# Kernel tuning notes

Hardware: AMD Instinct MI355X
Metric: run time of the kernel (lower is better)

The kernel has to match this reference:

```python
import jax, jax.numpy as jnp
import numpy as np

B, T, C = 4, 2048, 1024
H, HS = 16, 64


def setup_inputs() -> dict:
    key = jax.random.key(0)
    ks = jax.random.split(key, 5)
    scale = (H * C) ** (-0.5)
    x = jax.random.normal(ks[0], (B, T, C), dtype=jnp.float32)
    Wk = jax.random.normal(ks[1], (H, C, HS), dtype=jnp.float32) * scale
    Wq = jax.random.normal(ks[2], (H, C, HS), dtype=jnp.float32) * scale
    Wv = jax.random.normal(ks[3], (H, C, HS), dtype=jnp.float32) * scale
    proj_w = jax.random.normal(ks[4], (C, C), dtype=jnp.float32) / C ** 0.5
    proj_b = jnp.zeros((C,), dtype=jnp.float32)
    return {"x": x, "Wk": Wk, "Wq": Wq, "Wv": Wv, "proj_w": proj_w, "proj_b": proj_b}


def reference(x, Wk, Wq, Wv, proj_w, proj_b):
    b, t, c = x.shape
    # per-head projections: (B,T,C) x (H,C,D) -> (B,H,T,D)
    q = jnp.einsum('btc,hcd->bhtd', x, Wq)
    k = jnp.einsum('btc,hcd->bhtd', x, Wk)
    v = jnp.einsum('btc,hcd->bhtd', x, Wv)
    # NOTE: original module does not scale by 1/sqrt(head_size)
    wei = jnp.einsum('bhtd,bhsd->bhts', q, k)  # (B,H,T,T)
    causal = jnp.tril(jnp.ones((t, t), dtype=bool))
    wei = jnp.where(causal, wei, -jnp.inf)
    wei = jax.nn.softmax(wei, axis=-1)
    out = jnp.einsum('bhts,bhsd->bhtd', wei, v)
    out = out.transpose(0, 2, 1, 3).reshape(b, t, c)  # concat heads
    return out @ proj_w + proj_b
```

## Files before the change

kernel.cpp:

```cpp
#include <hip/hip_runtime.h>

typedef unsigned short u16;
typedef u16 u16x4 __attribute__((ext_vector_type(4)));
typedef u16 u16x8 __attribute__((ext_vector_type(8)));
typedef unsigned u32x2 __attribute__((ext_vector_type(2)));
typedef __bf16 bf16x8 __attribute__((ext_vector_type(8)));
typedef float f32x4 __attribute__((ext_vector_type(4)));

#define DEV static __device__ __forceinline__

DEV u16 f2bf(float f) {
  union { float f; unsigned u; } v; v.f = f;
  return (u16)((v.u + 0x7FFFu + ((v.u >> 16) & 1u)) >> 16);
}

DEV unsigned pack2(float a, float b) {
  unsigned ua = __builtin_bit_cast(unsigned, a) + 0x8000u;
  unsigned ub = __builtin_bit_cast(unsigned, b) + 0x8000u;
  return (ua >> 16) | (ub & 0xFFFF0000u);
}

DEV void async16(const void* g, void* l) {
  __builtin_amdgcn_global_load_lds((const __attribute__((address_space(1))) void*)g,
                                   (__attribute__((address_space(3))) void*)l, 16, 0, 0);
}

DEV f32x4 mfma16(bf16x8 a, bf16x8 b, f32x4 c) {
  return __builtin_amdgcn_mfma_f32_16x16x32_bf16(a, b, c, 0, 0, 0);
}

DEV float exp2fast(float x) { return __builtin_amdgcn_exp2f(x); }

#define BARRIER() asm volatile("s_barrier" ::: "memory")
#define SB0() __builtin_amdgcn_sched_barrier(0)

__global__ __launch_bounds__(256) void k_prep(const float* __restrict__ x,
                                              const float* __restrict__ Wk,
                                              const float* __restrict__ Wq,
                                              const float* __restrict__ Wv,
                                              const float* __restrict__ pw,
                                              u16* __restrict__ xb,
                                              u16* __restrict__ wT,
                                              u16* __restrict__ pwT) {
  __shared__ float t[64 * 72];
  const int bid = blockIdx.x, tid = threadIdx.x;
  if (bid < 8192) {
    int i = bid * 1024 + tid * 4;
    float4 v = *(const float4*)(x + i);
    u16x4 o = { f2bf(v.x), f2bf(v.y), f2bf(v.z), f2bf(v.w) };
    *(u16x4*)(xb + i) = o;
    return;
  }
  const int role = bid - 8192;
  const float* src;
  u16* dst;
  int rows, cols, bx, by, bz;
  float scale;
  if (role < 768) {
    const int w = role >> 8, rem = role & 255;
    src = (w == 0) ? Wq : ((w == 1) ? Wk : Wv);
    dst = wT + (size_t)w * 1024 * 1024;
    scale = (w == 0) ? 1.44269504088896340736f : 1.0f;
    rows = 1024; cols = 64; bx = 0; by = rem >> 4; bz = rem & 15;
  } else {
    const int p = role - 768;
    src = pw; dst = pwT; scale = 1.0f;
    rows = 1024; cols = 1024; bx = p & 15; by = p >> 4; bz = 0;
  }
  src += (size_t)bz * rows * cols;
  dst += (size_t)bz * rows * cols;
  const int c0 = bx * 64, r0 = by * 64;
  const int rr = tid >> 2, cb = (tid & 3) * 16;
  const float* s = src + (size_t)(r0 + rr) * cols + c0 + cb;
  float4 v0 = *(const float4*)(s + 0);
  float4 v1 = *(const float4*)(s + 4);
  float4 v2 = *(const float4*)(s + 8);
  float4 v3 = *(const float4*)(s + 12);
  *(float4*)(t + rr * 72 + cb + 0)  = v0;
  *(float4*)(t + rr * 72 + cb + 4)  = v1;
  *(float4*)(t + rr * 72 + cb + 8)  = v2;
  *(float4*)(t + rr * 72 + cb + 12) = v3;
  __syncthreads();
  const int dd = tid >> 2, eb = (tid & 3) * 16;
  u16x8 o0, o1;
#pragma unroll
  for (int e = 0; e < 8; ++e) o0[e] = f2bf(t[(eb + e) * 72 + dd] * scale);
#pragma unroll
  for (int e = 0; e < 8; ++e) o1[e] = f2bf(t[(eb + 8 + e) * 72 + dd] * scale);
  u16* dp = dst + (size_t)(c0 + dd) * rows + r0 + eb;
  *(u16x8*)dp = o0;
  *(u16x8*)(dp + 8) = o1;
}

template <int MODE>
__global__ __launch_bounds__(512, 2) void k_gemm(const u16* __restrict__ A,
                                                 const u16* __restrict__ Bt,
                                                 u16* __restrict__ qd,
                                                 u16* __restrict__ kd,
                                                 u16* __restrict__ vd,
                                                 float* __restrict__ out,
                                                 const float* __restrict__ bias) {
  __shared__ u16 lds[3 * 24576];
  const int tid = threadIdx.x;
  const int w = tid >> 6, lane = tid & 63;
  const int quad = lane >> 4, l15 = lane & 15;
  const int wm = w >> 1, wn = w & 1;

  const int gx = (int)gridDim.x;
  int lin = (int)blockIdx.y * gx + (int)blockIdx.x;
  const int nwg = gx * (int)gridDim.y;
  lin = (lin & 7) * (nwg >> 3) + (lin >> 3);
  const size_t mb = (size_t)(lin / gx);
  const int nb = lin % gx;

  const int lr = lane >> 3;
  const int lc = ((lane & 7) ^ lr) << 3;
  const u16* ga0 = A  + (mb * 256 + (size_t)(w * 8 + lr)) * 1024 + lc;
  const u16* gb0 = Bt + ((size_t)nb * 128 + (size_t)(w * 8 + lr)) * 1024 + lc;

  const int swz0 = ((0 + quad) ^ (l15 & 7)) << 3;
  const int swz1 = ((4 + quad) ^ (l15 & 7)) << 3;

  f32x4 acc[4][4] = {};

#pragma unroll
  for (int s2 = 0; s2 < 2; ++s2) {
    u16* d = lds + s2 * 24576 + w * 512;
#pragma unroll
    for (int g = 0; g < 4; ++g) async16(ga0 + (size_t)g * 65536 + s2 * 64, d + g * 4096);
#pragma unroll
    for (int g = 0; g < 2; ++g) async16(gb0 + (size_t)g * 65536 + s2 * 64, d + 16384 + g * 4096);
  }
  asm volatile("s_waitcnt vmcnt(6)" ::: "memory");
  BARRIER(); SB0();

#pragma unroll
  for (int s = 0; s < 16; ++s) {
    const u16* Ab = lds + (s % 3) * 24576;
    const u16* Bb = Ab + 16384;

    bf16x8 a0[4], b0[4];
#pragma unroll
    for (int i = 0; i < 4; ++i)
      a0[i] = *(const bf16x8*)(Ab + (wm * 64 + i * 16 + l15) * 64 + swz0);
#pragma unroll
    for (int j = 0; j < 4; ++j)
      b0[j] = *(const bf16x8*)(Bb + (wn * 64 + j * 16 + l15) * 64 + swz0);
    if (s < 14) {
      u16* d = lds + ((s + 2) % 3) * 24576 + w * 512;
      async16(ga0 + 0 * 65536 + (s + 2) * 64, d + 0 * 4096);
      async16(ga0 + 1 * 65536 + (s + 2) * 64, d + 1 * 4096);
      async16(ga0 + 2 * 65536 + (s + 2) * 64, d + 2 * 4096);
    }
    SB0(); BARRIER(); SB0();
    __builtin_amdgcn_s_setprio(1);
#pragma unroll
    for (int i = 0; i < 4; ++i)
#pragma unroll
      for (int j = 0; j < 4; ++j) acc[i][j] = mfma16(a0[i], b0[j], acc[i][j]);
    __builtin_amdgcn_s_setprio(0);
    SB0(); BARRIER(); SB0();

    bf16x8 a1[4], b1[4];
#pragma unroll
    for (int i = 0; i < 4; ++i)
      a1[i] = *(const bf16x8*)(Ab + (wm * 64 + i * 16 + l15) * 64 + swz1);
#pragma unroll
    for (int j = 0; j < 4; ++j)
      b1[j] = *(const bf16x8*)(Bb + (wn * 64 + j * 16 + l15) * 64 + swz1);
    if (s < 14) {
      u16* d = lds + ((s + 2) % 3) * 24576 + w * 512;
      async16(ga0 + 3 * 65536 + (s + 2) * 64, d + 3 * 4096);
      async16(gb0 + 0 * 65536 + (s + 2) * 64, d + 16384 + 0 * 4096);
      async16(gb0 + 1 * 65536 + (s + 2) * 64, d + 16384 + 4096);
    }
    SB0(); BARRIER(); SB0();
    __builtin_amdgcn_s_setprio(1);
#pragma unroll
    for (int i = 0; i < 4; ++i)
#pragma unroll
      for (int j = 0; j < 4; ++j) acc[i][j] = mfma16(a1[i], b1[j], acc[i][j]);
    __builtin_amdgcn_s_setprio(0);
    SB0();
    if (s < 14)       { asm volatile("s_waitcnt vmcnt(6)" ::: "memory"); }
    else if (s == 14) { asm volatile("s_waitcnt vmcnt(0)" ::: "memory"); }
    if (s < 15) { BARRIER(); SB0(); }
  }

  const size_t m0 = mb * 256 + wm * 64;
  const int n0 = nb * 128 + wn * 64;
  if (MODE == 0) {
#pragma unroll
    for (int j = 0; j < 4; ++j) {
      const int n = n0 + j * 16 + l15;
      const int p = n >> 10, hh = (n >> 6) & 15, d = n & 63;
      if (p == 2) {
#pragma unroll
        for (int i = 0; i < 4; ++i) {
          const size_t m = m0 + i * 16 + quad * 4;
          const size_t bb = m >> 11, tt = m & 2047;
          u16x4 pk = { f2bf(acc[i][j][0]), f2bf(acc[i][j][1]),
                       f2bf(acc[i][j][2]), f2bf(acc[i][j][3]) };
          *(u16x4*)(vd + ((bb * 16 + hh) * 64 + d) * 2048 + tt) = pk;
        }
      } else {
        u16* dst = (p == 0) ? qd : kd;
#pragma unroll
        for (int i = 0; i < 4; ++i)
#pragma unroll
          for (int r = 0; r < 4; ++r) {
            const size_t m = m0 + i * 16 + quad * 4 + r;
            const size_t bb = m >> 11, tt = m & 2047;
            dst[((bb * 16 + hh) * 2048 + tt) * 64 + d] = f2bf(acc[i][j][r]);
          }
      }
    }
  } else {
#pragma unroll
    for (int j = 0; j < 4; ++j) {
      const int n = n0 + j * 16 + l15;
      const float bv = bias[n];
#pragma unroll
      for (int i = 0; i < 4; ++i)
#pragma unroll
        for (int r = 0; r < 4; ++r) {
          const size_t m = m0 + i * 16 + quad * 4 + r;
          out[m * 1024 + n] = acc[i][j][r] + bv;
        }
    }
  }
}

__global__ __launch_bounds__(256) void k_attn(const u16* __restrict__ Qg,
                                              const u16* __restrict__ Kg,
                                              const u16* __restrict__ Vtg,
                                              u16* __restrict__ Og) {
  __shared__ u16 Kbuf[2 * 4096];
  __shared__ u16 Vbuf[2 * 4096];
  __shared__ u16 Pbuf[4 * 32 * 72];
  const int tid = threadIdx.x;
  const int wave = tid >> 6, lane = tid & 63;
  const int quad = lane >> 4, l15 = lane & 15;
  const int quad4 = quad * 4, quad8 = quad * 8;
  const int bh = blockIdx.x;
  const int qb = 15 - (int)blockIdx.y;
  const u16* kg = Kg + (size_t)bh * 2048 * 64;
  const u16* vg = Vtg + (size_t)bh * 64 * 2048;
  u16* Pw = Pbuf + wave * (32 * 72);
  const int b = bh >> 4, h = bh & 15;

  const int lrow = lane >> 3;
  const int lchunk = ((lane & 7) ^ lrow) << 3;
  const u16* kst = kg + (size_t)(wave * 16 + lrow) * 64 + lchunk;
  const u16* vst = vg + (size_t)(wave * 16 + lrow) * 2048 + lchunk;
  u16* kdst0 = Kbuf + wave * 1024;
  u16* vdst0 = Vbuf + wave * 1024;

  const int rowoff = l15 * 64;
  const int swz0 = ((0 + quad) ^ (l15 & 7)) << 3;
  const int swz1 = ((4 + quad) ^ (l15 & 7)) << 3;

  const int qlo = qb * 128 + wave * 32;
  const int ntw = 2 * qb + 1 + (wave >> 1);
  const int ntb = 2 * qb + 2;
  const u16* qg = Qg + ((size_t)bh * 2048 + (size_t)qb * 128) * 64;

  bf16x8 qf[2][2];
#pragma unroll
  for (int i = 0; i < 2; ++i)
#pragma unroll
    for (int c = 0; c < 2; ++c)
      qf[i][c] = *(const bf16x8*)(qg + (size_t)(wave * 32 + i * 16 + l15) * 64 +
                                  c * 32 + quad8);

  f32x4 oacc[2][4] = {};
  float lsum[2] = {0.f, 0.f};
  const f32x4 fzero = {};

  async16(kst, kdst0);
  async16(kst + 512, kdst0 + 512);
  async16(vst, vdst0);
  async16(vst + 16384, vdst0 + 512);

  for (int it = 0; it < ntb; ++it) {
    __syncthreads();

    if (it + 1 < ntb) {
      const int buf = (it + 1) & 1;
      const size_t s0n = (size_t)(it + 1) * 64;
      async16(kst + s0n * 64,       kdst0 + buf * 4096);
      async16(kst + s0n * 64 + 512, kdst0 + buf * 4096 + 512);
      async16(vst + s0n,            vdst0 + buf * 4096);
      async16(vst + s0n + 16384,    vdst0 + buf * 4096 + 512);
    }

    if (it < ntw) {
      const int s0 = it * 64;
      const u16* Kb = Kbuf + (it & 1) * 4096;
      const u16* Vb = Vbuf + (it & 1) * 4096;

      f32x4 sacc[4][2];
#pragma unroll
      for (int j = 0; j < 4; ++j) {
        bf16x8 kf0 = *(const bf16x8*)(Kb + j * 1024 + rowoff + swz0);
        bf16x8 kf1 = *(const bf16x8*)(Kb + j * 1024 + rowoff + swz1);
        sacc[j][0] = mfma16(kf0, qf[0][0], fzero);
        sacc[j][0] = mfma16(kf1, qf[0][1], sacc[j][0]);
        sacc[j][1] = mfma16(kf0, qf[1][0], fzero);
        sacc[j][1] = mfma16(kf1, qf[1][1], sacc[j][1]);
      }

#pragma unroll
      for (int j = 0; j < 4; ++j)
#pragma unroll
        for (int i = 0; i < 2; ++i)
#pragma unroll
          for (int r = 0; r < 4; ++r)
            sacc[j][i][r] = exp2fast(sacc[j][i][r]);

      if (it == ntw - 1) {
#pragma unroll
        for (int j = 0; j < 4; ++j)
#pragma unroll
          for (int i = 0; i < 2; ++i)
#pragma unroll
            for (int r = 0; r < 4; ++r)
              if (s0 + j * 16 + quad4 + r > qlo + i * 16 + l15) sacc[j][i][r] = 0.f;
      }

#pragma unroll
      for (int j = 0; j < 4; ++j)
#pragma unroll
        for (int i = 0; i < 2; ++i) {
          lsum[i] += (sacc[j][i][0] + sacc[j][i][1]) +
                     (sacc[j][i][2] + sacc[j][i][3]);
          u32x2 pk = { pack2(sacc[j][i][0], sacc[j][i][1]),
                       pack2(sacc[j][i][2], sacc[j][i][3]) };
          *(u32x2*)(Pw + (i * 16 + l15) * 72 + j * 16 + quad4) = pk;
        }

      bf16x8 pa[2][2];
#pragma unroll
      for (int i = 0; i < 2; ++i)
#pragma unroll
        for (int c = 0; c < 2; ++c)
          pa[i][c] = *(const bf16x8*)(Pw + (i * 16 + l15) * 72 + c * 32 + quad8);

#pragma unroll
      for (int n = 0; n < 4; ++n) {
        bf16x8 vf0 = *(const bf16x8*)(Vb + n * 1024 + rowoff + swz0);
        bf16x8 vf1 = *(const bf16x8*)(Vb + n * 1024 + rowoff + swz1);
        oacc[0][n] = mfma16(pa[0][0], vf0, oacc[0][n]);
        oacc[0][n] = mfma16(pa[0][1], vf1, oacc[0][n]);
        oacc[1][n] = mfma16(pa[1][0], vf0, oacc[1][n]);
        oacc[1][n] = mfma16(pa[1][1], vf1, oacc[1][n]);
      }
    }
  }

#pragma unroll
  for (int i = 0; i < 2; ++i) {
    lsum[i] += __shfl_xor(lsum[i], 16, 64);
    lsum[i] += __shfl_xor(lsum[i], 32, 64);
  }
#pragma unroll
  for (int i = 0; i < 2; ++i)
#pragma unroll
    for (int r = 0; r < 4; ++r) {
      const float inv = 1.0f / __shfl(lsum[i], quad4 + r, 16);
      const size_t t = (size_t)qb * 128 + wave * 32 + i * 16 + quad4 + r;
#pragma unroll
      for (int n = 0; n < 4; ++n)
        Og[((size_t)b * 2048 + t) * 1024 + h * 64 + n * 16 + l15] =
            f2bf(oacc[i][n][r] * inv);
    }
}

extern "C" void kernel_launch(void* const* d_in, const int* in_sizes, int n_in,
                              void* d_out, int out_size, void* d_ws, size_t ws_size,
                              hipStream_t stream) {
  const float* x  = (const float*)d_in[0];
  const float* Wk = (const float*)d_in[1];
  const float* Wq = (const float*)d_in[2];
  const float* Wv = (const float*)d_in[3];
  const float* pw = (const float*)d_in[4];
  const float* pb = (const float*)d_in[5];
  float* out = (float*)d_out;
  char* ws = (char*)d_ws;

  u16* xb  = (u16*)(ws + 0);
  u16* wT  = (u16*)(ws + 16777216);
  u16* pwT = (u16*)(ws + 23068672);
  u16* q   = (u16*)(ws + 25165824);
  u16* kb  = (u16*)(ws + 41943040);
  u16* vt  = (u16*)(ws + 58720256);
  u16* att = (u16*)(ws + 0);

  k_prep<<<9216, 256, 0, stream>>>(x, Wk, Wq, Wv, pw, xb, wT, pwT);
  k_gemm<0><<<dim3(24, 32), 512, 0, stream>>>(xb, wT, q, kb, vt, nullptr, nullptr);
  k_attn<<<dim3(64, 16), 256, 0, stream>>>(q, kb, vt, att);
  k_gemm<1><<<dim3(8, 32), 512, 0, stream>>>(att, pwT, nullptr, nullptr, nullptr, out, pb);
}
```

Measured before the change: 241.7 us.

## Compute softmax row sums via MFMA with ones, use native bf16 convert, set priorities

Removes the per-element scalar accumulation of the softmax denominator and instead computes row sums with extra MFMAs that multiply the bf16 P tiles by a ones vector. As a side effect the sums now match the rounded bf16 P values used in the PV product. The manual pack2 rounding is replaced with native bf16 conversions, and s_setprio is raised around the MFMA blocks to favour matrix issue across waves. This adds four MFMAs per tile in exchange for fewer VALU adds and no final cross-lane shuffles.

After: 242.0 us. No clear change (+0.2%).

```diff
diff --git a/kernel.cpp b/kernel.cpp
--- a/kernel.cpp
+++ b/kernel.cpp
@@ -4,6 +4,7 @@
 typedef u16 u16x4 __attribute__((ext_vector_type(4)));
 typedef u16 u16x8 __attribute__((ext_vector_type(8)));
 typedef unsigned u32x2 __attribute__((ext_vector_type(2)));
+typedef __bf16 bf16x4 __attribute__((ext_vector_type(4)));
 typedef __bf16 bf16x8 __attribute__((ext_vector_type(8)));
 typedef float f32x4 __attribute__((ext_vector_type(4)));
 
@@ -12,12 +13,6 @@
 DEV u16 f2bf(float f) {
   union { float f; unsigned u; } v; v.f = f;
   return (u16)((v.u + 0x7FFFu + ((v.u >> 16) & 1u)) >> 16);
-}
-
-DEV unsigned pack2(float a, float b) {
-  unsigned ua = __builtin_bit_cast(unsigned, a) + 0x8000u;
-  unsigned ub = __builtin_bit_cast(unsigned, b) + 0x8000u;
-  return (ua >> 16) | (ub & 0xFFFF0000u);
 }
 
 DEV void async16(const void* g, void* l) {
@@ -274,8 +269,11 @@
                                   c * 32 + quad8);
 
   f32x4 oacc[2][4] = {};
-  float lsum[2] = {0.f, 0.f};
+  f32x4 lacc[2] = {};
   const f32x4 fzero = {};
+  const u16x8 onesu = {0x3F80, 0x3F80, 0x3F80, 0x3F80,
+                       0x3F80, 0x3F80, 0x3F80, 0x3F80};
+  const bf16x8 onesf = __builtin_bit_cast(bf16x8, onesu);
 
   async16(kst, kdst0);
   async16(kst + 512, kdst0 + 512);
@@ -300,6 +298,7 @@
       const u16* Vb = Vbuf + (it & 1) * 4096;
 
       f32x4 sacc[4][2];
+      __builtin_amdgcn_s_setprio(1);
 #pragma unroll
       for (int j = 0; j < 4; ++j) {
         bf16x8 kf0 = *(const bf16x8*)(Kb + j * 1024 + rowoff + swz0);
@@ -309,6 +308,7 @@
         sacc[j][1] = mfma16(kf0, qf[1][0], fzero);
         sacc[j][1] = mfma16(kf1, qf[1][1], sacc[j][1]);
       }
+      __builtin_amdgcn_s_setprio(0);
 
 #pragma unroll
       for (int j = 0; j < 4; ++j)
@@ -332,11 +332,9 @@
       for (int j = 0; j < 4; ++j)
 #pragma unroll
         for (int i = 0; i < 2; ++i) {
-          lsum[i] += (sacc[j][i][0] + sacc[j][i][1]) +
-                     (sacc[j][i][2] + sacc[j][i][3]);
-          u32x2 pk = { pack2(sacc[j][i][0], sacc[j][i][1]),
-                       pack2(sacc[j][i][2], sacc[j][i][3]) };
-          *(u32x2*)(Pw + (i * 16 + l15) * 72 + j * 16 + quad4) = pk;
+          bf16x4 pk = { (__bf16)sacc[j][i][0], (__bf16)sacc[j][i][1],
+                        (__bf16)sacc[j][i][2], (__bf16)sacc[j][i][3] };
+          *(bf16x4*)(Pw + (i * 16 + l15) * 72 + j * 16 + quad4) = pk;
         }
 
       bf16x8 pa[2][2];
@@ -346,6 +344,7 @@
         for (int c = 0; c < 2; ++c)
           pa[i][c] = *(const bf16x8*)(Pw + (i * 16 + l15) * 72 + c * 32 + quad8);
 
+      __builtin_amdgcn_s_setprio(1);
 #pragma unroll
       for (int n = 0; n < 4; ++n) {
         bf16x8 vf0 = *(const bf16x8*)(Vb + n * 1024 + rowoff + swz0);
@@ -355,19 +354,19 @@
         oacc[1][n] = mfma16(pa[1][0], vf0, oacc[1][n]);
         oacc[1][n] = mfma16(pa[1][1], vf1, oacc[1][n]);
       }
-    }
-  }
-
-#pragma unroll
-  for (int i = 0; i < 2; ++i) {
-    lsum[i] += __shfl_xor(lsum[i], 16, 64);
-    lsum[i] += __shfl_xor(lsum[i], 32, 64);
-  }
+      lacc[0] = mfma16(pa[0][0], onesf, lacc[0]);
+      lacc[0] = mfma16(pa[0][1], onesf, lacc[0]);
+      lacc[1] = mfma16(pa[1][0], onesf, lacc[1]);
+      lacc[1] = mfma16(pa[1][1], onesf, lacc[1]);
+      __builtin_amdgcn_s_setprio(0);
+    }
+  }
+
 #pragma unroll
   for (int i = 0; i < 2; ++i)
 #pragma unroll
     for (int r = 0; r < 4; ++r) {
-      const float inv = 1.0f / __shfl(lsum[i], quad4 + r, 16);
+      const float inv = 1.0f / lacc[i][r];
       const size_t t = (size_t)qb * 128 + wave * 32 + i * 16 + quad4 + r;
 #pragma unroll
       for (int n = 0; n < 4; ++n)
```
